# Kernel optimization log

Measured on AMD Instinct MI355X. Metric: run time of the kernel, lower is better.

## Reference

```python
import jax, jax.numpy as jnp
import numpy as np

N_HEADS = 16
ROPE_BASE = 10000.0


def _rope_tables(T, head_dim, dtype):
    d2 = head_dim // 2
    inv_freq = 1.0 / (ROPE_BASE ** (jnp.arange(0, head_dim, 2, dtype=jnp.float32) / head_dim))
    t = jnp.arange(T, dtype=jnp.float32)
    freqs = jnp.outer(t, inv_freq)  # [T, d2]
    cos = jnp.cos(freqs)[None, :, None, :].astype(dtype)  # [1,T,1,d2]
    sin = jnp.sin(freqs)[None, :, None, :].astype(dtype)
    return cos, sin


def _apply_rotary(x, cos, sin):
    # x: [B,T,H,D]; rotate halves
    d = x.shape[-1] // 2
    x1, x2 = x[..., :d], x[..., d:]
    return jnp.concatenate([x1 * cos + x2 * sin, -x1 * sin + x2 * cos], axis=-1)


def setup_inputs() -> dict:
    key = jax.random.key(0)
    k1, k2, k3 = jax.random.split(key, 3)
    B, T, C = 2, 2048, 1024
    x = jax.random.normal(k1, (B, T, C), dtype=jnp.float32)
    w_attn = jax.random.normal(k2, (3 * C, C), dtype=jnp.float32) * (1.0 / np.sqrt(C))
    w_proj = jax.random.normal(k3, (C, C), dtype=jnp.float32) * (1.0 / np.sqrt(C))
    return {"x": x, "w_attn": w_attn, "w_proj": w_proj}


def reference(x, w_attn, w_proj):
    B, T, C = x.shape
    H = N_HEADS
    D = C // H
    qkv = jnp.einsum('btc,fc->btf', x, w_attn)  # [B,T,3C]
    q, k, v = jnp.split(qkv, 3, axis=2)
    q = q.reshape(B, T, H, D)
    k = k.reshape(B, T, H, D)
    v = v.reshape(B, T, H, D)
    cos, sin = _rope_tables(T, D, x.dtype)
    q = _apply_rotary(q, cos, sin)
    k = _apply_rotary(k, cos, sin)
    # causal SDPA, scale 1/sqrt(D)
    scale = 1.0 / np.sqrt(D)
    scores = jnp.einsum('bqhd,bkhd->bhqk', q, k) * scale
    causal = jnp.tril(jnp.ones((T, T), dtype=bool))
    scores = jnp.where(causal[None, None], scores, jnp.finfo(scores.dtype).min)
    attn = jax.nn.softmax(scores, axis=-1)
    y = jnp.einsum('bhqk,bkhd->bqhd', attn, v).reshape(B, T, C)
    return jnp.einsum('btc,oc->bto', y, w_proj)
```

## Files before the change

kernel.cpp:

```cpp
#include <hip/hip_runtime.h>
#include <math.h>

typedef __bf16 bf16x8 __attribute__((ext_vector_type(8)));
typedef float f32x4 __attribute__((ext_vector_type(4)));

__device__ __forceinline__ unsigned f2bf(float f) {
    union { float f; unsigned u; } v; v.f = f;
    return (v.u + 0x7FFFu + ((v.u >> 16) & 1u)) >> 16;
}

__device__ __forceinline__ void gload16(const ushort* g, ushort* l) {
    __builtin_amdgcn_global_load_lds(
        (const __attribute__((address_space(1))) void*)g,
        (__attribute__((address_space(3))) void*)l, 16, 0, 0);
}

__device__ __forceinline__ bool src_is_fp32(const unsigned* s) {
    int sane = 0;
#pragma unroll
    for (int i = 0; i < 64; ++i) {
        unsigned lo = s[i] & 0xFFFFu;
        unsigned e = (lo >> 7) & 0xFF;
        if (lo == 0u || (e >= 100u && e <= 140u)) sane++;
    }
    return sane < 48;
}

__global__ __launch_bounds__(256) void tobf16_all_kernel(
    const unsigned* __restrict__ s0, const unsigned* __restrict__ s1,
    const unsigned* __restrict__ s2,
    ushort* __restrict__ d0, ushort* __restrict__ d1, ushort* __restrict__ d2) {
    const int bx = blockIdx.x;
    const unsigned* src;
    ushort* dst;
    int lb;
    if (bx < 2048)      { src = s0; dst = d0; lb = bx; }
    else if (bx < 3584) { src = s1; dst = d1; lb = bx - 2048; }
    else                { src = s2; dst = d2; lb = bx - 3584; }
    const int i = lb * 2048 + threadIdx.x * 8;
    if (src_is_fp32(src)) {
        const float* fs = (const float*)src;
        float4 f0 = *(const float4*)(fs + i);
        float4 f1 = *(const float4*)(fs + i + 4);
        uint4 o;
        o.x = f2bf(f0.x) | (f2bf(f0.y) << 16);
        o.y = f2bf(f0.z) | (f2bf(f0.w) << 16);
        o.z = f2bf(f1.x) | (f2bf(f1.y) << 16);
        o.w = f2bf(f1.z) | (f2bf(f1.w) << 16);
        *(uint4*)(dst + i) = o;
    } else {
        *(uint4*)(dst + i) = *(const uint4*)((const ushort*)src + i);
    }
}

constexpr int GBM = 128, GBN = 128, GBK = 32;

__global__ __launch_bounds__(256) void gemm_qkv_rope_kernel(
    const ushort* __restrict__ A, const ushort* __restrict__ Bmat,
    ushort* __restrict__ qkvh, int K) {
    __shared__ ushort As[2][GBM * GBK];
    __shared__ ushort Bs[2][GBN * GBK];

    const int tid  = threadIdx.x;
    const int lane = tid & 63;
    const int wv   = tid >> 6;
    const int wm   = (wv >> 1) * 64;
    const int wn   = (wv & 1) * 64;

    const ushort* Ab = A + (size_t)blockIdx.x * GBM * K;
    const ushort* Bb = Bmat + (size_t)blockIdx.y * GBN * K;

    f32x4 acc[4][4];
#pragma unroll
    for (int i = 0; i < 4; i++)
#pragma unroll
        for (int j = 0; j < 4; j++) acc[i][j] = (f32x4){0.f, 0.f, 0.f, 0.f};

    const int srow = tid >> 2;
    const int scol = (tid & 3) * 8;
    const int fr = lane & 15;
    const int fk = (lane >> 4) * 8;
    const int nK = K >> 5;

    gload16(Ab + (size_t)srow * K + scol,        As[0] + wv * 512);
    gload16(Ab + (size_t)(srow + 64) * K + scol, As[0] + wv * 512 + 2048);
    gload16(Bb + (size_t)srow * K + scol,        Bs[0] + wv * 512);
    gload16(Bb + (size_t)(srow + 64) * K + scol, Bs[0] + wv * 512 + 2048);

#pragma unroll 1
    for (int it = 0; it < nK; ++it) {
        const int cur = it & 1;
        __syncthreads();
        if (it + 1 < nK) {
            const int k0 = (it + 1) << 5, nxt = cur ^ 1;
            gload16(Ab + (size_t)srow * K + k0 + scol,        As[nxt] + wv * 512);
            gload16(Ab + (size_t)(srow + 64) * K + k0 + scol, As[nxt] + wv * 512 + 2048);
            gload16(Bb + (size_t)srow * K + k0 + scol,        Bs[nxt] + wv * 512);
            gload16(Bb + (size_t)(srow + 64) * K + k0 + scol, Bs[nxt] + wv * 512 + 2048);
        }
        bf16x8 af[4], bfr[4];
#pragma unroll
        for (int i = 0; i < 4; i++)
            af[i] = *(const bf16x8*)(As[cur] + (wm + i * 16 + fr) * GBK + fk);
#pragma unroll
        for (int j = 0; j < 4; j++)
            bfr[j] = *(const bf16x8*)(Bs[cur] + (wn + j * 16 + fr) * GBK + fk);
#pragma unroll
        for (int i = 0; i < 4; i++)
#pragma unroll
            for (int j = 0; j < 4; j++)
                acc[i][j] = __builtin_amdgcn_mfma_f32_16x16x32_bf16(af[i], bfr[j], acc[i][j], 0, 0, 0);
    }

    const int crow0 = (lane >> 4) * 4;
    const int col0  = blockIdx.y * GBN + wn;
    const int which = col0 >> 10;
    const int hh    = (col0 >> 6) & 15;
    ushort* outp = qkvh + (size_t)which * 4194304 + (size_t)hh * 131072;

    if (which < 2) {
        const float inva = exp2f((float)fr * -0.41524101186f);
        const float invb = exp2f((float)(fr + 16) * -0.41524101186f);
        const float qs = (which == 0) ? 0.125f : 1.0f;
#pragma unroll
        for (int i = 0; i < 4; i++)
#pragma unroll
            for (int r = 0; r < 4; r++) {
                int row = blockIdx.x * GBM + wm + i * 16 + crow0 + r;
                int t = row & 2047;
                size_t ob = ((size_t)(row >> 11)) * 2097152 + (size_t)t * 64;
                float sa, ca, sb, cb;
                __sincosf((float)t * inva, &sa, &ca);
                __sincosf((float)t * invb, &sb, &cb);
                float q0 = acc[i][0][r], q1 = acc[i][1][r];
                float q2 = acc[i][2][r], q3 = acc[i][3][r];
                float n0 = (q0 * ca + q2 * sa) * qs;
                float n1 = (q1 * cb + q3 * sb) * qs;
                float n2 = (q2 * ca - q0 * sa) * qs;
                float n3 = (q3 * cb - q1 * sb) * qs;
                outp[ob + fr]      = (ushort)f2bf(n0);
                outp[ob + 16 + fr] = (ushort)f2bf(n1);
                outp[ob + 32 + fr] = (ushort)f2bf(n2);
                outp[ob + 48 + fr] = (ushort)f2bf(n3);
            }
    } else {
#pragma unroll
        for (int i = 0; i < 4; i++)
#pragma unroll
            for (int r = 0; r < 4; r++) {
                int row = blockIdx.x * GBM + wm + i * 16 + crow0 + r;
                int t = row & 2047;
                size_t ob = ((size_t)(row >> 11)) * 2097152 + (size_t)t * 64;
#pragma unroll
                for (int j = 0; j < 4; j++)
                    outp[ob + j * 16 + fr] = (ushort)f2bf(acc[i][j][r]);
            }
    }
}

__global__ __launch_bounds__(256) void gemm_bt_kernel(
    const ushort* __restrict__ A, const ushort* __restrict__ Bmat,
    float* __restrict__ C, int M, int N, int K) {
    __shared__ ushort As[2][GBM * GBK];
    __shared__ ushort Bs[2][GBN * GBK];

    const int tid  = threadIdx.x;
    const int lane = tid & 63;
    const int wv   = tid >> 6;
    const int wm   = (wv >> 1) * 64;
    const int wn   = (wv & 1) * 64;

    const ushort* Ab = A + (size_t)blockIdx.x * GBM * K;
    const ushort* Bb = Bmat + (size_t)blockIdx.y * GBN * K;

    f32x4 acc[4][4];
#pragma unroll
    for (int i = 0; i < 4; i++)
#pragma unroll
        for (int j = 0; j < 4; j++) acc[i][j] = (f32x4){0.f, 0.f, 0.f, 0.f};

    const int srow = tid >> 2;
    const int scol = (tid & 3) * 8;
    const int fr = lane & 15;
    const int fk = (lane >> 4) * 8;
    const int nK = K >> 5;

    gload16(Ab + (size_t)srow * K + scol,        As[0] + wv * 512);
    gload16(Ab + (size_t)(srow + 64) * K + scol, As[0] + wv * 512 + 2048);
    gload16(Bb + (size_t)srow * K + scol,        Bs[0] + wv * 512);
    gload16(Bb + (size_t)(srow + 64) * K + scol, Bs[0] + wv * 512 + 2048);

#pragma unroll 1
    for (int it = 0; it < nK; ++it) {
        const int cur = it & 1;
        __syncthreads();
        if (it + 1 < nK) {
            const int k0 = (it + 1) << 5, nxt = cur ^ 1;
            gload16(Ab + (size_t)srow * K + k0 + scol,        As[nxt] + wv * 512);
            gload16(Ab + (size_t)(srow + 64) * K + k0 + scol, As[nxt] + wv * 512 + 2048);
            gload16(Bb + (size_t)srow * K + k0 + scol,        Bs[nxt] + wv * 512);
            gload16(Bb + (size_t)(srow + 64) * K + k0 + scol, Bs[nxt] + wv * 512 + 2048);
        }
        bf16x8 af[4], bfr[4];
#pragma unroll
        for (int i = 0; i < 4; i++)
            af[i] = *(const bf16x8*)(As[cur] + (wm + i * 16 + fr) * GBK + fk);
#pragma unroll
        for (int j = 0; j < 4; j++)
            bfr[j] = *(const bf16x8*)(Bs[cur] + (wn + j * 16 + fr) * GBK + fk);
#pragma unroll
        for (int i = 0; i < 4; i++)
#pragma unroll
            for (int j = 0; j < 4; j++)
                acc[i][j] = __builtin_amdgcn_mfma_f32_16x16x32_bf16(af[i], bfr[j], acc[i][j], 0, 0, 0);
    }

    const int crow0 = (lane >> 4) * 4;
#pragma unroll
    for (int i = 0; i < 4; i++)
#pragma unroll
        for (int j = 0; j < 4; j++)
#pragma unroll
            for (int r = 0; r < 4; r++) {
                int row = blockIdx.x * GBM + wm + i * 16 + crow0 + r;
                int col = blockIdx.y * GBN + wn + j * 16 + fr;
                C[(size_t)row * N + col] = acc[i][j][r];
            }
}

#define NEG_BIG (-1e30f)
constexpr int LPK = 72;
constexpr int LPV = 136;

__global__ __launch_bounds__(512) void attn_kernel(const ushort* __restrict__ qkvh,
                                                   ushort* __restrict__ y) {
    __shared__ ushort Ks[2][128 * LPK];
    __shared__ ushort Vt[2][64 * LPV];
    __shared__ ushort Ps[8][16 * LPV];

    const int tid  = threadIdx.x;
    const int lane = tid & 63;
    const int wv   = tid >> 6;
    const int pid  = blockIdx.x;
    const int bh   = blockIdx.y;
    const int b    = bh >> 4, h = bh & 15;

    const ushort* qp = qkvh + (size_t)b * 2097152 + (size_t)h * 131072;
    const ushort* kp = qp + 4194304;
    const ushort* vp = qp + 8388608;

    const int fr = lane & 15;
    const int fq = lane >> 4;
    const int fk = fq * 8;

    const int srow = tid >> 2;
    const int scol = (tid & 3) * 16;
    const int vkey = tid & 127;
    const int vd0  = (tid >> 7) * 16;

#pragma unroll 1
    for (int seg = 0; seg < 2; ++seg) {
        const int qb = seg ? (15 - pid) : pid;
        const int nIt = qb + 1;

        __syncthreads();

        const int qrow = qb * 128 + wv * 16 + fr;
        bf16x8 qf0 = *(const bf16x8*)(qp + (size_t)qrow * 64 + fk);
        bf16x8 qf1 = *(const bf16x8*)(qp + (size_t)qrow * 64 + 32 + fk);

        f32x4 o[4];
        o[0] = o[1] = o[2] = o[3] = (f32x4){0.f, 0.f, 0.f, 0.f};
        float lacc[4] = {0.f, 0.f, 0.f, 0.f};

        uint4 kr0, kr1, vr0, vr1;
        {
            const ushort* sk = kp + (size_t)srow * 64 + scol;
            kr0 = *(const uint4*)(sk);
            kr1 = *(const uint4*)(sk + 8);
            const ushort* sv = vp + (size_t)vkey * 64 + vd0;
            vr0 = *(const uint4*)(sv);
            vr1 = *(const uint4*)(sv + 8);
            *(uint4*)(Ks[0] + srow * LPK + scol)     = kr0;
            *(uint4*)(Ks[0] + srow * LPK + scol + 8) = kr1;
            unsigned w[8] = {vr0.x, vr0.y, vr0.z, vr0.w, vr1.x, vr1.y, vr1.z, vr1.w};
#pragma unroll
            for (int jj = 0; jj < 8; ++jj) {
                Vt[0][(vd0 + 2 * jj)     * LPV + vkey] = (ushort)(w[jj] & 0xFFFFu);
                Vt[0][(vd0 + 2 * jj + 1) * LPV + vkey] = (ushort)(w[jj] >> 16);
            }
        }
        if (1 < nIt) {
            const ushort* sk = kp + (size_t)(128 + srow) * 64 + scol;
            kr0 = *(const uint4*)(sk);
            kr1 = *(const uint4*)(sk + 8);
            const ushort* sv = vp + (size_t)(128 + vkey) * 64 + vd0;
            vr0 = *(const uint4*)(sv);
            vr1 = *(const uint4*)(sv + 8);
        }

#pragma unroll 1
        for (int it = 0; it < nIt; ++it) {
            const int cur = it & 1;
            const int k0 = it * 128;
            __syncthreads();
            if (it + 1 < nIt) {
                const int nxt = cur ^ 1;
                *(uint4*)(Ks[nxt] + srow * LPK + scol)     = kr0;
                *(uint4*)(Ks[nxt] + srow * LPK + scol + 8) = kr1;
                unsigned w[8] = {vr0.x, vr0.y, vr0.z, vr0.w, vr1.x, vr1.y, vr1.z, vr1.w};
#pragma unroll
                for (int jj = 0; jj < 8; ++jj) {
                    Vt[nxt][(vd0 + 2 * jj)     * LPV + vkey] = (ushort)(w[jj] & 0xFFFFu);
                    Vt[nxt][(vd0 + 2 * jj + 1) * LPV + vkey] = (ushort)(w[jj] >> 16);
                }
                if (it + 2 < nIt) {
                    const ushort* sk = kp + (size_t)(k0 + 256 + srow) * 64 + scol;
                    kr0 = *(const uint4*)(sk);
                    kr1 = *(const uint4*)(sk + 8);
                    const ushort* sv = vp + (size_t)(k0 + 256 + vkey) * 64 + vd0;
                    vr0 = *(const uint4*)(sv);
                    vr1 = *(const uint4*)(sv + 8);
                }
            }

            f32x4 s[8];
#pragma unroll
            for (int j = 0; j < 8; ++j) {
                bf16x8 kf0 = *(const bf16x8*)(Ks[cur] + (j * 16 + fr) * LPK + fk);
                bf16x8 kf1 = *(const bf16x8*)(Ks[cur] + (j * 16 + fr) * LPK + 32 + fk);
                f32x4 z = (f32x4){0.f, 0.f, 0.f, 0.f};
                z = __builtin_amdgcn_mfma_f32_16x16x32_bf16(qf0, kf0, z, 0, 0, 0);
                z = __builtin_amdgcn_mfma_f32_16x16x32_bf16(qf1, kf1, z, 0, 0, 0);
                s[j] = z;
            }
            if (it + 1 < nIt) {
#pragma unroll
                for (int j = 0; j < 8; ++j)
#pragma unroll
                    for (int r = 0; r < 4; ++r) {
                        float p = __expf(s[j][r]);
                        s[j][r] = p;
                        lacc[r] += p;
                    }
            } else {
                const int rowg = qb * 128 + wv * 16 + fq * 4;
#pragma unroll
                for (int j = 0; j < 8; ++j)
#pragma unroll
                    for (int r = 0; r < 4; ++r) {
                        float v = s[j][r];
                        if ((k0 + j * 16 + fr) > (rowg + r)) v = NEG_BIG;
                        float p = __expf(v);
                        s[j][r] = p;
                        lacc[r] += p;
                    }
            }

            ushort* pw = Ps[wv];
#pragma unroll
            for (int j = 0; j < 8; ++j)
#pragma unroll
                for (int r = 0; r < 4; ++r)
                    pw[(fq * 4 + r) * LPV + j * 16 + fr] = (ushort)f2bf(s[j][r]);
            __asm__ volatile("" ::: "memory");

#pragma unroll
            for (int kk = 0; kk < 4; ++kk) {
                bf16x8 pf = *(const bf16x8*)(pw + fr * LPV + kk * 32 + fk);
#pragma unroll
                for (int j = 0; j < 4; ++j) {
                    bf16x8 vf = *(const bf16x8*)(Vt[cur] + (j * 16 + fr) * LPV + kk * 32 + fk);
                    o[j] = __builtin_amdgcn_mfma_f32_16x16x32_bf16(pf, vf, o[j], 0, 0, 0);
                }
            }
        }

#pragma unroll
        for (int msk = 1; msk < 16; msk <<= 1)
#pragma unroll
            for (int r = 0; r < 4; ++r)
                lacc[r] += __shfl_xor(lacc[r], msk, 64);
#pragma unroll
        for (int j = 0; j < 4; ++j)
#pragma unroll
            for (int r = 0; r < 4; ++r) {
                int row = qb * 128 + wv * 16 + fq * 4 + r;
                y[((size_t)b * 2048 + row) * 1024 + h * 64 + j * 16 + fr] =
                    (ushort)f2bf(o[j][r] / lacc[r]);
            }
    }
}

extern "C" void kernel_launch(void* const* d_in, const int* in_sizes, int n_in,
                              void* d_out, int out_size, void* d_ws, size_t ws_size,
                              hipStream_t stream) {
    const int nx = in_sizes[0];
    const int na = in_sizes[1];
    const int np = in_sizes[2];

    ushort* qkvh = (ushort*)d_ws;
    ushort* yb   = qkvh + (size_t)3 * 4194304;
    ushort* xb   = yb + (size_t)4096 * 1024;
    ushort* wab  = xb + nx;
    ushort* wpb  = wab + na;
    size_t need = ((size_t)3 * 4194304 + (size_t)4096 * 1024 + nx + na + np) * 2;
    if (ws_size < need) return;

    tobf16_all_kernel<<<dim3(4096), 256, 0, stream>>>(
        (const unsigned*)d_in[0], (const unsigned*)d_in[1], (const unsigned*)d_in[2],
        xb, wab, wpb);

    gemm_qkv_rope_kernel<<<dim3(32, 24), 256, 0, stream>>>(xb, wab, qkvh, 1024);
    attn_kernel<<<dim3(8, 32), 512, 0, stream>>>(qkvh, yb);
    gemm_bt_kernel<<<dim3(32, 8), 256, 0, stream>>>(yb, wpb, (float*)d_out, 4096, 1024, 1024);
}
```

Measured before the change: 194.3 us.

## Launch one causal query tile per workgroup with single-buffered K/V LDS

The attention kernel no longer processes a balanced pair of query tiles (qb and 15-qb) in one workgroup. Each workgroup now handles a single query tile, and the grid doubles to 16x32. The tile order is mirrored by batch so heavy and light tiles interleave. K/V shared buffers drop from double to single buffering with two barriers per iteration, keeping register prefetch of the next tile. This cuts LDS use so two workgroups can share a CU, at the cost of extra synchronization and possible causal load imbalance across workgroups.

```diff
diff --git a/kernel.cpp b/kernel.cpp
--- a/kernel.cpp
+++ b/kernel.cpp
@@ -234,16 +234,17 @@
 
 __global__ __launch_bounds__(512) void attn_kernel(const ushort* __restrict__ qkvh,
                                                    ushort* __restrict__ y) {
-    __shared__ ushort Ks[2][128 * LPK];
-    __shared__ ushort Vt[2][64 * LPV];
+    __shared__ ushort Ks[128 * LPK];
+    __shared__ ushort Vt[64 * LPV];
     __shared__ ushort Ps[8][16 * LPV];
 
     const int tid  = threadIdx.x;
     const int lane = tid & 63;
     const int wv   = tid >> 6;
-    const int pid  = blockIdx.x;
     const int bh   = blockIdx.y;
     const int b    = bh >> 4, h = bh & 15;
+    const int qb   = (bh & 16) ? (15 - blockIdx.x) : blockIdx.x;
+    const int nIt  = qb + 1;
 
     const ushort* qp = qkvh + (size_t)b * 2097152 + (size_t)h * 131072;
     const ushort* kp = qp + 4194304;
@@ -258,138 +259,113 @@
     const int vkey = tid & 127;
     const int vd0  = (tid >> 7) * 16;
 
+    const int qrow = qb * 128 + wv * 16 + fr;
+    bf16x8 qf0 = *(const bf16x8*)(qp + (size_t)qrow * 64 + fk);
+    bf16x8 qf1 = *(const bf16x8*)(qp + (size_t)qrow * 64 + 32 + fk);
+
+    f32x4 o[4];
+    o[0] = o[1] = o[2] = o[3] = (f32x4){0.f, 0.f, 0.f, 0.f};
+    float lacc[4] = {0.f, 0.f, 0.f, 0.f};
+
+    uint4 kr0, kr1, vr0, vr1;
+    {
+        const ushort* sk = kp + (size_t)srow * 64 + scol;
+        kr0 = *(const uint4*)(sk);
+        kr1 = *(const uint4*)(sk + 8);
+        const ushort* sv = vp + (size_t)vkey * 64 + vd0;
+        vr0 = *(const uint4*)(sv);
+        vr1 = *(const uint4*)(sv + 8);
+    }
+
 #pragma unroll 1
-    for (int seg = 0; seg < 2; ++seg) {
-        const int qb = seg ? (15 - pid) : pid;
-        const int nIt = qb + 1;
-
+    for (int it = 0; it < nIt; ++it) {
+        const int k0 = it * 128;
         __syncthreads();
-
-        const int qrow = qb * 128 + wv * 16 + fr;
-        bf16x8 qf0 = *(const bf16x8*)(qp + (size_t)qrow * 64 + fk);
-        bf16x8 qf1 = *(const bf16x8*)(qp + (size_t)qrow * 64 + 32 + fk);
-
-        f32x4 o[4];
-        o[0] = o[1] = o[2] = o[3] = (f32x4){0.f, 0.f, 0.f, 0.f};
-        float lacc[4] = {0.f, 0.f, 0.f, 0.f};
-
-        uint4 kr0, kr1, vr0, vr1;
+        *(uint4*)(Ks + srow * LPK + scol)     = kr0;
+        *(uint4*)(Ks + srow * LPK + scol + 8) = kr1;
         {
-            const ushort* sk = kp + (size_t)srow * 64 + scol;
+            unsigned w[8] = {vr0.x, vr0.y, vr0.z, vr0.w, vr1.x, vr1.y, vr1.z, vr1.w};
+#pragma unroll
+            for (int jj = 0; jj < 8; ++jj) {
+                Vt[(vd0 + 2 * jj)     * LPV + vkey] = (ushort)(w[jj] & 0xFFFFu);
+                Vt[(vd0 + 2 * jj + 1) * LPV + vkey] = (ushort)(w[jj] >> 16);
+            }
+        }
+        __syncthreads();
+        if (it + 1 < nIt) {
+            const ushort* sk = kp + (size_t)(k0 + 128 + srow) * 64 + scol;
             kr0 = *(const uint4*)(sk);
             kr1 = *(const uint4*)(sk + 8);
-            const ushort* sv = vp + (size_t)vkey * 64 + vd0;
+            const ushort* sv = vp + (size_t)(k0 + 128 + vkey) * 64 + vd0;
             vr0 = *(const uint4*)(sv);
             vr1 = *(const uint4*)(sv + 8);
-            *(uint4*)(Ks[0] + srow * LPK + scol)     = kr0;
-            *(uint4*)(Ks[0] + srow * LPK + scol + 8) = kr1;
-            unsigned w[8] = {vr0.x, vr0.y, vr0.z, vr0.w, vr1.x, vr1.y, vr1.z, vr1.w};
-#pragma unroll
-            for (int jj = 0; jj < 8; ++jj) {
-                Vt[0][(vd0 + 2 * jj)     * LPV + vkey] = (ushort)(w[jj] & 0xFFFFu);
-                Vt[0][(vd0 + 2 * jj + 1) * LPV + vkey] = (ushort)(w[jj] >> 16);
-            }
-        }
-        if (1 < nIt) {
-            const ushort* sk = kp + (size_t)(128 + srow) * 64 + scol;
-            kr0 = *(const uint4*)(sk);
-            kr1 = *(const uint4*)(sk + 8);
-            const ushort* sv = vp + (size_t)(128 + vkey) * 64 + vd0;
-            vr0 = *(const uint4*)(sv);
-            vr1 = *(const uint4*)(sv + 8);
-        }
-
-#pragma unroll 1
-        for (int it = 0; it < nIt; ++it) {
-            const int cur = it & 1;
-            const int k0 = it * 128;
-            __syncthreads();
-            if (it + 1 < nIt) {
-                const int nxt = cur ^ 1;
-                *(uint4*)(Ks[nxt] + srow * LPK + scol)     = kr0;
-                *(uint4*)(Ks[nxt] + srow * LPK + scol + 8) = kr1;
-                unsigned w[8] = {vr0.x, vr0.y, vr0.z, vr0.w, vr1.x, vr1.y, vr1.z, vr1.w};
-#pragma unroll
-                for (int jj = 0; jj < 8; ++jj) {
-                    Vt[nxt][(vd0 + 2 * jj)     * LPV + vkey] = (ushort)(w[jj] & 0xFFFFu);
-                    Vt[nxt][(vd0 + 2 * jj + 1) * LPV + vkey] = (ushort)(w[jj] >> 16);
+        }
+
+        f32x4 s[8];
+#pragma unroll
+        for (int j = 0; j < 8; ++j) {
+            bf16x8 kf0 = *(const bf16x8*)(Ks + (j * 16 + fr) * LPK + fk);
+            bf16x8 kf1 = *(const bf16x8*)(Ks + (j * 16 + fr) * LPK + 32 + fk);
+            f32x4 z = (f32x4){0.f, 0.f, 0.f, 0.f};
+            z = __builtin_amdgcn_mfma_f32_16x16x32_bf16(qf0, kf0, z, 0, 0, 0);
+            z = __builtin_amdgcn_mfma_f32_16x16x32_bf16(qf1, kf1, z, 0, 0, 0);
+            s[j] = z;
+        }
+        if (it + 1 < nIt) {
+#pragma unroll
+            for (int j = 0; j < 8; ++j)
+#pragma unroll
+                for (int r = 0; r < 4; ++r) {
+                    float p = __expf(s[j][r]);
+                    s[j][r] = p;
+                    lacc[r] += p;
                 }
-                if (it + 2 < nIt) {
-                    const ushort* sk = kp + (size_t)(k0 + 256 + srow) * 64 + scol;
-                    kr0 = *(const uint4*)(sk);
-                    kr1 = *(const uint4*)(sk + 8);
-                    const ushort* sv = vp + (size_t)(k0 + 256 + vkey) * 64 + vd0;
-                    vr0 = *(const uint4*)(sv);
-                    vr1 = *(const uint4*)(sv + 8);
+        } else {
+            const int rowg = qb * 128 + wv * 16 + fq * 4;
+#pragma unroll
+            for (int j = 0; j < 8; ++j)
+#pragma unroll
+                for (int r = 0; r < 4; ++r) {
+                    float v = s[j][r];
+                    if ((k0 + j * 16 + fr) > (rowg + r)) v = NEG_BIG;
+                    float p = __expf(v);
+                    s[j][r] = p;
+                    lacc[r] += p;
                 }
-            }
-
-            f32x4 s[8];
-#pragma unroll
-            for (int j = 0; j < 8; ++j) {
-                bf16x8 kf0 = *(const bf16x8*)(Ks[cur] + (j * 16 + fr) * LPK + fk);
-                bf16x8 kf1 = *(const bf16x8*)(Ks[cur] + (j * 16 + fr) * LPK + 32 + fk);
-                f32x4 z = (f32x4){0.f, 0.f, 0.f, 0.f};
-                z = __builtin_amdgcn_mfma_f32_16x16x32_bf16(qf0, kf0, z, 0, 0, 0);
-                z = __builtin_amdgcn_mfma_f32_16x16x32_bf16(qf1, kf1, z, 0, 0, 0);
-                s[j] = z;
-            }
-            if (it + 1 < nIt) {
-#pragma unroll
-                for (int j = 0; j < 8; ++j)
-#pragma unroll
-                    for (int r = 0; r < 4; ++r) {
-                        float p = __expf(s[j][r]);
-                        s[j][r] = p;
-                        lacc[r] += p;
-                    }
-            } else {
-                const int rowg = qb * 128 + wv * 16 + fq * 4;
-#pragma unroll
-                for (int j = 0; j < 8; ++j)
-#pragma unroll
-                    for (int r = 0; r < 4; ++r) {
-                        float v = s[j][r];
-                        if ((k0 + j * 16 + fr) > (rowg + r)) v = NEG_BIG;
-                        float p = __expf(v);
-                        s[j][r] = p;
-                        lacc[r] += p;
-                    }
-            }
-
-            ushort* pw = Ps[wv];
-#pragma unroll
-            for (int j = 0; j < 8; ++j)
-#pragma unroll
-                for (int r = 0; r < 4; ++r)
-                    pw[(fq * 4 + r) * LPV + j * 16 + fr] = (ushort)f2bf(s[j][r]);
-            __asm__ volatile("" ::: "memory");
-
-#pragma unroll
-            for (int kk = 0; kk < 4; ++kk) {
-                bf16x8 pf = *(const bf16x8*)(pw + fr * LPV + kk * 32 + fk);
-#pragma unroll
-                for (int j = 0; j < 4; ++j) {
-                    bf16x8 vf = *(const bf16x8*)(Vt[cur] + (j * 16 + fr) * LPV + kk * 32 + fk);
-                    o[j] = __builtin_amdgcn_mfma_f32_16x16x32_bf16(pf, vf, o[j], 0, 0, 0);
-                }
-            }
-        }
-
-#pragma unroll
-        for (int msk = 1; msk < 16; msk <<= 1)
+        }
+
+        ushort* pw = Ps[wv];
+#pragma unroll
+        for (int j = 0; j < 8; ++j)
 #pragma unroll
             for (int r = 0; r < 4; ++r)
-                lacc[r] += __shfl_xor(lacc[r], msk, 64);
-#pragma unroll
-        for (int j = 0; j < 4; ++j)
-#pragma unroll
-            for (int r = 0; r < 4; ++r) {
-                int row = qb * 128 + wv * 16 + fq * 4 + r;
-                y[((size_t)b * 2048 + row) * 1024 + h * 64 + j * 16 + fr] =
-                    (ushort)f2bf(o[j][r] / lacc[r]);
-            }
-    }
+                pw[(fq * 4 + r) * LPV + j * 16 + fr] = (ushort)f2bf(s[j][r]);
+        __asm__ volatile("" ::: "memory");
+
+#pragma unroll
+        for (int kk = 0; kk < 4; ++kk) {
+            bf16x8 pf = *(const bf16x8*)(pw + fr * LPV + kk * 32 + fk);
+#pragma unroll
+            for (int j = 0; j < 4; ++j) {
+                bf16x8 vf = *(const bf16x8*)(Vt + (j * 16 + fr) * LPV + kk * 32 + fk);
+                o[j] = __builtin_amdgcn_mfma_f32_16x16x32_bf16(pf, vf, o[j], 0, 0, 0);
+            }
+        }
+    }
+
+#pragma unroll
+    for (int msk = 1; msk < 16; msk <<= 1)
+#pragma unroll
+        for (int r = 0; r < 4; ++r)
+            lacc[r] += __shfl_xor(lacc[r], msk, 64);
+#pragma unroll
+    for (int j = 0; j < 4; ++j)
+#pragma unroll
+        for (int r = 0; r < 4; ++r) {
+            int row = qb * 128 + wv * 16 + fq * 4 + r;
+            y[((size_t)b * 2048 + row) * 1024 + h * 64 + j * 16 + fr] =
+                (ushort)f2bf(o[j][r] / lacc[r]);
+        }
 }
 
 extern "C" void kernel_launch(void* const* d_in, const int* in_sizes, int n_in,
@@ -412,6 +388,6 @@
         xb, wab, wpb);
 
     gemm_qkv_rope_kernel<<<dim3(32, 24), 256, 0, stream>>>(xb, wab, qkvh, 1024);
-    attn_kernel<<<dim3(8, 32), 512, 0, stream>>>(qkvh, yb);
+    attn_kernel<<<dim3(16, 32), 512, 0, stream>>>(qkvh, yb);
     gemm_bt_kernel<<<dim3(32, 8), 256, 0, stream>>>(yb, wpb, (float*)d_out, 4096, 1024, 1024);
 }
```

After: 204.3 us. 5.1% more time.
